# Kernel tuning notes

Measured on AMD Instinct MI355X. Metric: run time of the kernel, lower is better.

## Reference

```python
import jax, jax.numpy as jnp
import numpy as np

N_NODES = 50000
N_EDGES = 800000
DIM = 128
HEADS = 8
DK = DIM // HEADS  # 16
SQRT_DK = float(np.sqrt(DK))


def setup_inputs() -> dict:
    key = jax.random.key(0)
    ks = jax.random.split(key, 12)
    inp = {
        "h": jax.random.normal(ks[0], (N_NODES, DIM), jnp.float32),
        "src": jax.random.randint(ks[1], (N_EDGES,), 0, N_NODES, jnp.int32),
        "dst": jax.random.randint(ks[2], (N_EDGES,), 0, N_NODES, jnp.int32),
        "Wk": jax.random.normal(ks[3], (DIM, DIM), jnp.float32) / np.sqrt(DIM),
        "bk": jnp.zeros((DIM,), jnp.float32),
        "Wq": jax.random.normal(ks[4], (DIM, DIM), jnp.float32) / np.sqrt(DIM),
        "bq": jnp.zeros((DIM,), jnp.float32),
        "Wv": jax.random.normal(ks[5], (DIM, DIM), jnp.float32) / np.sqrt(DIM),
        "bv": jnp.zeros((DIM,), jnp.float32),
        "Wa": jax.random.normal(ks[6], (DIM, DIM), jnp.float32) / np.sqrt(DIM),
        "ba": jnp.zeros((DIM,), jnp.float32),
        "rel_att": jax.random.normal(ks[7], (HEADS, DK, DK), jnp.float32) / np.sqrt(DK),
        "rel_msg": jax.random.normal(ks[8], (HEADS, DK, DK), jnp.float32) / np.sqrt(DK),
        "rel_pri": jnp.ones((HEADS,), jnp.float32),
        "skip": jnp.ones((1,), jnp.float32),
    }
    return inp


def reference(h, src, dst, Wk, bk, Wq, bq, Wv, bv, Wa, ba, rel_att, rel_msg, rel_pri, skip):
    N = h.shape[0]
    # node-level projections -> [N, H, d_k]
    k = (h @ Wk + bk).reshape(N, HEADS, DK)
    q = (h @ Wq + bq).reshape(N, HEADS, DK)
    v = (h @ Wv + bv).reshape(N, HEADS, DK)
    # relation-specific transforms
    k = jnp.einsum('nhi,hij->nhj', k, rel_att)
    v = jnp.einsum('nhi,hij->nhj', v, rel_msg)
    # per-edge score: dot(q[dst], k[src]) over d_k -> [E, H]
    score = jnp.einsum('ehd,ehd->eh', q[dst], k[src]) * rel_pri / SQRT_DK
    # segment softmax over destination nodes (edge_softmax, norm_by='dst')
    smax = jax.ops.segment_max(score, dst, num_segments=N)  # [N, H]
    e = jnp.exp(score - smax[dst])
    ssum = jax.ops.segment_sum(e, dst, num_segments=N)  # [N, H]
    attn = e / ssum[dst]  # [E, H]
    # weighted scatter-sum of messages: sum_e v[src_e] * attn_e -> [N, H, d_k]
    m = v[src] * attn[:, :, None]
    t = jax.ops.segment_sum(m, dst, num_segments=N).reshape(N, DIM)
    # target-specific aggregation (dropout in eval mode = identity, use_norm=False)
    trans_out = t @ Wa + ba
    alpha = jax.nn.sigmoid(skip)  # [1], broadcasts
    new_h = trans_out * alpha + h * (1.0 - alpha)
    return new_h
```

## Files before the change

### kernel.cpp

```cpp
#include <hip/hip_runtime.h>
#include <stdint.h>

#define NN 50000
#define NE 800000

typedef __bf16 v8bf __attribute__((ext_vector_type(8)));
typedef float  v4f  __attribute__((ext_vector_type(4)));
typedef unsigned short v8us __attribute__((ext_vector_type(8)));

#define EXP2F(x) __builtin_amdgcn_exp2f(x)

__device__ __forceinline__ float bf2f(unsigned short u) {
    return __uint_as_float(((unsigned)u) << 16);
}
__device__ __forceinline__ unsigned short f2bf(float f) {
    unsigned u = __float_as_uint(f);
    u += 0x7FFFu + ((u >> 16) & 1u);
    return (unsigned short)(u >> 16);
}
__device__ __forceinline__ float ldf(const void* p, size_t i, int isb) {
    return isb ? bf2f(((const unsigned short*)p)[i]) : ((const float*)p)[i];
}
__device__ __forceinline__ unsigned uminu(unsigned a, unsigned b) {
    return a < b ? a : b;
}

__global__ __launch_bounds__(128) void k_prep(
    const void* __restrict__ Wq, const void* __restrict__ bq,
    const void* __restrict__ Wk, const void* __restrict__ bk,
    const void* __restrict__ Wv, const void* __restrict__ bv,
    const void* __restrict__ Wa, const void* __restrict__ ba,
    const void* __restrict__ rel_att, const void* __restrict__ rel_msg,
    const void* __restrict__ rel_pri, const int* __restrict__ dst,
    unsigned* __restrict__ CNTP, unsigned short* __restrict__ RANKS,
    int* __restrict__ FLAG, unsigned short* __restrict__ WTb,
    float* __restrict__ BC)
{
    int b = blockIdx.x;
    int j = threadIdx.x;
    if (b >= 512) {
        int e = (b - 512) * 128 + j;
        unsigned r = atomicAdd(&CNTP[(unsigned)dst[e] << 4], 1u);
        RANKS[e] = (unsigned short)r;
        return;
    }
    const unsigned rp0 = ((const unsigned*)rel_pri)[0];
    const int isb = ((rp0 & 0xFFFFu) != 0u) ? 1 : 0;
    int m = b >> 7;
    int i = b & 127;
    if (b == 0 && j == 0) FLAG[0] = isb;
    if (m == 0) {
        WTb[((size_t)(0 * 128 + j)) * 128 + i] = f2bf(ldf(Wq, i * 128 + j, isb));
        if (i == 0) BC[j] = ldf(bq, j, isb);
    } else if (m == 3) {
        WTb[((size_t)(3 * 128 + j)) * 128 + i] = f2bf(ldf(Wa, i * 128 + j, isb));
        if (i == 0) BC[3 * 128 + j] = ldf(ba, j, isb);
    } else {
        const void* W    = (m == 1) ? Wk : Wv;
        const void* bias = (m == 1) ? bk : bv;
        const void* R    = (m == 1) ? rel_att : rel_msg;
        int hh = j >> 4, jj = j & 15;
        float scale = (m == 1) ? ldf(rel_pri, hh, isb) * 0.25f : 1.0f;
        float acc = 0.f, bacc = 0.f;
        #pragma unroll
        for (int l = 0; l < 16; ++l) {
            float r = ldf(R, hh * 256 + l * 16 + jj, isb);
            acc  += ldf(W, i * 128 + hh * 16 + l, isb) * r;
            bacc += ldf(bias, hh * 16 + l, isb) * r;
        }
        WTb[((size_t)(m * 128 + j)) * 128 + i] = f2bf(acc * scale);
        if (i == 0) BC[m * 128 + j] = bacc * scale;
    }
}

#define NBG 391
#define NSB 98
__global__ __launch_bounds__(256, 2) void k_qkvscan(
    const void* __restrict__ h, const unsigned short* __restrict__ WTb,
    const float* __restrict__ BC, const int* __restrict__ FLAG,
    unsigned short* __restrict__ Qb, unsigned short* __restrict__ KVb,
    const unsigned* __restrict__ CNTP,
    unsigned* __restrict__ RPS, unsigned* __restrict__ BSUM,
    unsigned* __restrict__ BOFF, unsigned* __restrict__ DONE)
{
    __shared__ __align__(16) unsigned short Ah[128][136];
    __shared__ __align__(16) unsigned short Bh[128][136];
    __shared__ int lastFlag;
    const int tid = threadIdx.x;

    if (blockIdx.x >= NBG) {
        unsigned* shs = (unsigned*)&Ah[0][0];
        int sb = blockIdx.x - NBG;
        int g0 = sb * 512 + tid * 2, g1 = g0 + 1;
        unsigned v0 = (g0 < NN) ? CNTP[(size_t)g0 << 4] : 0u;
        unsigned v1 = (g1 < NN) ? CNTP[(size_t)g1 << 4] : 0u;
        unsigned pv = v0 + v1;
        shs[tid] = pv;
        __syncthreads();
        #pragma unroll
        for (int off = 1; off < 256; off <<= 1) {
            unsigned t = 0;
            if (tid >= off) t = shs[tid - off];
            __syncthreads();
            if (tid >= off) shs[tid] += t;
            __syncthreads();
        }
        unsigned excl = shs[tid] - pv;
        if (g0 < NN) RPS[g0] = excl;
        if (g1 < NN) RPS[g1] = excl + v0;
        if (tid == 255) atomicExch(&BSUM[sb], shs[255]);
        __syncthreads();
        if (tid == 0) {
            __threadfence();
            lastFlag = (atomicAdd(DONE, 1u) == NSB - 1);
        }
        __syncthreads();
        if (!lastFlag) return;
        unsigned bv = (tid < NSB) ? atomicAdd(&BSUM[tid], 0u) : 0u;
        __syncthreads();
        shs[tid] = bv;
        __syncthreads();
        #pragma unroll
        for (int off = 1; off < 256; off <<= 1) {
            unsigned t = 0;
            if (tid >= off) t = shs[tid - off];
            __syncthreads();
            if (tid >= off) shs[tid] += t;
            __syncthreads();
        }
        if (tid < NSB) BOFF[tid] = shs[tid] - bv;
        return;
    }

    const int isb = FLAG[0];
    const int rowBase = blockIdx.x * 128;

    if (isb) {
        #pragma unroll
        for (int i = 0; i < 8; ++i) {
            int lin = tid + i * 256;
            int row = lin >> 4, kc = (lin & 15) * 8;
            int gr = rowBase + row;
            uint4 u = make_uint4(0, 0, 0, 0);
            if (gr < NN) u = *(const uint4*)((const unsigned short*)h + (size_t)gr * 128 + kc);
            *(uint4*)&Ah[row][kc] = u;
        }
    } else {
        #pragma unroll
        for (int i = 0; i < 16; ++i) {
            int lin = tid + i * 256;
            int row = lin >> 5, c4 = (lin & 31) * 4;
            int gr = rowBase + row;
            ushort4 o = make_ushort4(0, 0, 0, 0);
            if (gr < NN) {
                float4 f = *(const float4*)((const float*)h + (size_t)gr * 128 + c4);
                o.x = f2bf(f.x); o.y = f2bf(f.y); o.z = f2bf(f.z); o.w = f2bf(f.w);
            }
            *(ushort4*)&Ah[row][c4] = o;
        }
    }

    const int w = tid >> 6, l = tid & 63;
    const int lr = l & 15, q = l >> 4;
    v4f accK[2][8];

    for (int m = 0; m < 3; ++m) {
        if (m) __syncthreads();
        #pragma unroll
        for (int i = 0; i < 8; ++i) {
            int lin = tid + i * 256;
            int col = lin >> 4, kc = (lin & 15) * 8;
            uint4 u = *(const uint4*)(WTb + ((size_t)(m * 128 + col)) * 128 + kc);
            *(uint4*)&Bh[col][kc] = u;
        }
        __syncthreads();

        v4f acc[2][8];
        #pragma unroll
        for (int rt = 0; rt < 2; ++rt)
            #pragma unroll
            for (int nt = 0; nt < 8; ++nt) {
                float bj = BC[m * 128 + nt * 16 + lr];
                acc[rt][nt] = (v4f){bj, bj, bj, bj};
            }
        #pragma unroll
        for (int kk = 0; kk < 4; ++kk) {
            v8bf a0 = *(const v8bf*)&Ah[w * 32 +  0 + lr][kk * 32 + q * 8];
            v8bf a1 = *(const v8bf*)&Ah[w * 32 + 16 + lr][kk * 32 + q * 8];
            #pragma unroll
            for (int nt = 0; nt < 8; ++nt) {
                v8bf b = *(const v8bf*)&Bh[nt * 16 + lr][kk * 32 + q * 8];
                acc[0][nt] = __builtin_amdgcn_mfma_f32_16x16x32_bf16(a0, b, acc[0][nt], 0, 0, 0);
                acc[1][nt] = __builtin_amdgcn_mfma_f32_16x16x32_bf16(a1, b, acc[1][nt], 0, 0, 0);
            }
        }
        if (m == 0) {
            #pragma unroll
            for (int rt = 0; rt < 2; ++rt)
                #pragma unroll
                for (int nt = 0; nt < 8; ++nt)
                    #pragma unroll
                    for (int r = 0; r < 4; ++r) {
                        int row = rowBase + w * 32 + rt * 16 + q * 4 + r;
                        if (row < NN)
                            Qb[(size_t)row * 128 + nt * 16 + lr] = f2bf(acc[rt][nt][r]);
                    }
        } else if (m == 1) {
            #pragma unroll
            for (int rt = 0; rt < 2; ++rt)
                #pragma unroll
                for (int nt = 0; nt < 8; ++nt) accK[rt][nt] = acc[rt][nt];
        } else {
            #pragma unroll
            for (int rt = 0; rt < 2; ++rt)
                #pragma unroll
                for (int nt = 0; nt < 8; ++nt)
                    #pragma unroll
                    for (int r = 0; r < 4; ++r) {
                        int row = rowBase + w * 32 + rt * 16 + q * 4 + r;
                        if (row < NN) {
                            ushort2 kv;
                            kv.x = f2bf(accK[rt][nt][r]);
                            kv.y = f2bf(acc[rt][nt][r]);
                            *(ushort2*)&KVb[(size_t)row * 256 + (nt * 16 + lr) * 2] = kv;
                        }
                    }
        }
    }
}

__global__ __launch_bounds__(256) void k_fill(
    const int* __restrict__ src, const int* __restrict__ dst,
    const unsigned short* __restrict__ RANKS,
    const unsigned* __restrict__ RPS, const unsigned* __restrict__ BOFF,
    unsigned short* __restrict__ ESRC, unsigned* __restrict__ ROW)
{
    int t = blockIdx.x * 256 + threadIdx.x;
    if (t < NN) ROW[t] = RPS[t] + BOFF[t >> 9];
    if (t >= NE / 2) return;
    int e = t * 2;
    const int2 d2 = *(const int2*)(dst + e);
    const int2 s2 = *(const int2*)(src + e);
    const ushort2 r2 = *(const ushort2*)(RANKS + e);
    unsigned p0 = RPS[d2.x] + BOFF[d2.x >> 9] + r2.x;
    unsigned p1 = RPS[d2.y] + BOFF[d2.y >> 9] + r2.y;
    ESRC[p0] = (unsigned short)s2.x;
    ESRC[p1] = (unsigned short)s2.y;
}

__global__ __launch_bounds__(256) void k_attn(
    const unsigned* __restrict__ ROW,
    const unsigned short* __restrict__ ESRC,
    const unsigned short* __restrict__ Qb, const unsigned short* __restrict__ KVb,
    unsigned short* __restrict__ Tb)
{
    int d = (blockIdx.x * 256 + threadIdx.x) >> 6;
    int lane = threadIdx.x & 63;
    int hl = lane >> 5;
    int sub = lane & 31;
    const float LOG2E = 1.4426950408889634f;

    unsigned beg = ROW[d];
    unsigned end = (d == NN - 1) ? (unsigned)NE : ROW[d + 1];

    const ushort4 qu = *(const ushort4*)(Qb + (size_t)d * 128 + sub * 4);
    float q0 = bf2f(qu.x) * LOG2E, q1 = bf2f(qu.y) * LOG2E;
    float q2 = bf2f(qu.z) * LOG2E, q3 = bf2f(qu.w) * LOG2E;

    float s = 0.f, o0 = 0.f, o1 = 0.f, o2 = 0.f, o3 = 0.f;
    int n = (int)(end - beg);

#define ATT_F(kv) {                                                         \
        float p = q0 * bf2f(kv[0]) + q1 * bf2f(kv[2])                       \
                + q2 * bf2f(kv[4]) + q3 * bf2f(kv[6]);                      \
        p += __shfl_xor(p, 1);                                              \
        p += __shfl_xor(p, 2);                                              \
        float wgt = EXP2F(p);                                               \
        s  += wgt;                                                          \
        o0 += wgt * bf2f(kv[1]); o1 += wgt * bf2f(kv[3]);                   \
        o2 += wgt * bf2f(kv[5]); o3 += wgt * bf2f(kv[7]); }
#define ATT_T(kv, idx) {                                                    \
        float p = q0 * bf2f(kv[0]) + q1 * bf2f(kv[2])                       \
                + q2 * bf2f(kv[4]) + q3 * bf2f(kv[6]);                      \
        p += __shfl_xor(p, 1);                                              \
        p += __shfl_xor(p, 2);                                              \
        float wgt = ((idx) < end) ? EXP2F(p) : 0.f;                         \
        s  += wgt;                                                          \
        o0 += wgt * bf2f(kv[1]); o1 += wgt * bf2f(kv[3]);                   \
        o2 += wgt * bf2f(kv[5]); o3 += wgt * bf2f(kv[7]); }
#define GATH(sid) (*(const v8us*)(KVB + (((unsigned)(sid) << 9) + voff)))

    if (n > 0) {
        const unsigned char* KVB = (const unsigned char*)KVb;
        const unsigned voff = (unsigned)(sub * 16);
        const unsigned last = end - 1;
        const int RT = (n + 7) >> 3;
        const int tail = n & 7;
        const unsigned b0 = beg + (unsigned)hl;

        unsigned sA0 = ESRC[uminu(b0 + 0u, last)];
        unsigned sA1 = ESRC[uminu(b0 + 2u, last)];
        unsigned sA2 = ESRC[uminu(b0 + 4u, last)];
        unsigned sA3 = ESRC[uminu(b0 + 6u, last)];
        v8us kA0 = GATH(sA0), kA1 = GATH(sA1), kA2 = GATH(sA2), kA3 = GATH(sA3);
        unsigned sB0 = 0, sB1 = 0, sB2 = 0, sB3 = 0;
        if (RT > 1) {
            unsigned b1 = b0 + 8u;
            sB0 = ESRC[uminu(b1 + 0u, last)];
            sB1 = ESRC[uminu(b1 + 2u, last)];
            sB2 = ESRC[uminu(b1 + 4u, last)];
            sB3 = ESRC[uminu(b1 + 6u, last)];
        }

        for (int r = 0; r < RT; ++r) {
            v8us kB0 = kA0, kB1 = kA1, kB2 = kA2, kB3 = kA3;
            if (r + 1 < RT) {
                kB0 = GATH(sB0); kB1 = GATH(sB1);
                kB2 = GATH(sB2); kB3 = GATH(sB3);
            }
            unsigned sC0 = sB0, sC1 = sB1, sC2 = sB2, sC3 = sB3;
            if (r + 2 < RT) {
                unsigned b2 = b0 + (unsigned)(8 * (r + 2));
                sC0 = ESRC[uminu(b2 + 0u, last)];
                sC1 = ESRC[uminu(b2 + 2u, last)];
                sC2 = ESRC[uminu(b2 + 4u, last)];
                sC3 = ESRC[uminu(b2 + 6u, last)];
            }
            if (r == RT - 1 && tail) {
                unsigned base = beg + (unsigned)(8 * r) + (unsigned)hl;
                ATT_T(kA0, base + 0u);
                ATT_T(kA1, base + 2u);
                ATT_T(kA2, base + 4u);
                ATT_T(kA3, base + 6u);
            } else {
                ATT_F(kA0); ATT_F(kA1); ATT_F(kA2); ATT_F(kA3);
            }
            kA0 = kB0; kA1 = kB1; kA2 = kB2; kA3 = kB3;
            sB0 = sC0; sB1 = sC1; sB2 = sC2; sB3 = sC3;
        }
    }
#undef ATT_F
#undef ATT_T
#undef GATH

    s  += __shfl_xor(s, 32);
    o0 += __shfl_xor(o0, 32);
    o1 += __shfl_xor(o1, 32);
    o2 += __shfl_xor(o2, 32);
    o3 += __shfl_xor(o3, 32);
    float r = (s > 0.f) ? (1.0f / s) : 0.f;
    if (hl == 0) {
        ushort4 o;
        o.x = f2bf(o0 * r); o.y = f2bf(o1 * r);
        o.z = f2bf(o2 * r); o.w = f2bf(o3 * r);
        *(ushort4*)(Tb + (size_t)d * 128 + sub * 4) = o;
    }
}

__global__ __launch_bounds__(256, 2) void k_final_m(
    const unsigned short* __restrict__ Tb, const unsigned short* __restrict__ WTb,
    const float* __restrict__ BC, const void* __restrict__ h,
    const void* __restrict__ skip, const int* __restrict__ FLAG,
    void* __restrict__ out)
{
    __shared__ __align__(16) unsigned short Ah[128][136];
    __shared__ __align__(16) unsigned short Bh[128][136];
    const int isb = FLAG[0];
    const int tid = threadIdx.x;
    const int rowBase = blockIdx.x * 128;

    #pragma unroll
    for (int i = 0; i < 8; ++i) {
        int lin = tid + i * 256;
        int row = lin >> 4, kc = (lin & 15) * 8;
        int gr = rowBase + row;
        uint4 u = make_uint4(0, 0, 0, 0);
        if (gr < NN) u = *(const uint4*)(Tb + (size_t)gr * 128 + kc);
        *(uint4*)&Ah[row][kc] = u;
    }
    #pragma unroll
    for (int i = 0; i < 8; ++i) {
        int lin = tid + i * 256;
        int col = lin >> 4, kc = (lin & 15) * 8;
        uint4 u = *(const uint4*)(WTb + ((size_t)(3 * 128 + col)) * 128 + kc);
        *(uint4*)&Bh[col][kc] = u;
    }
    __syncthreads();

    const int w = tid >> 6, l = tid & 63;
    const int lr = l & 15, q = l >> 4;
    v4f acc[2][8];
    #pragma unroll
    for (int rt = 0; rt < 2; ++rt)
        #pragma unroll
        for (int nt = 0; nt < 8; ++nt) {
            float bj = BC[3 * 128 + nt * 16 + lr];
            acc[rt][nt] = (v4f){bj, bj, bj, bj};
        }
    #pragma unroll
    for (int kk = 0; kk < 4; ++kk) {
        v8bf a0 = *(const v8bf*)&Ah[w * 32 +  0 + lr][kk * 32 + q * 8];
        v8bf a1 = *(const v8bf*)&Ah[w * 32 + 16 + lr][kk * 32 + q * 8];
        #pragma unroll
        for (int nt = 0; nt < 8; ++nt) {
            v8bf b = *(const v8bf*)&Bh[nt * 16 + lr][kk * 32 + q * 8];
            acc[0][nt] = __builtin_amdgcn_mfma_f32_16x16x32_bf16(a0, b, acc[0][nt], 0, 0, 0);
            acc[1][nt] = __builtin_amdgcn_mfma_f32_16x16x32_bf16(a1, b, acc[1][nt], 0, 0, 0);
        }
    }
    float skipv = ldf(skip, 0, isb);
    float alpha = 1.0f / (1.0f + __expf(-skipv));
    float beta = 1.0f - alpha;
    #pragma unroll
    for (int rt = 0; rt < 2; ++rt)
        #pragma unroll
        for (int nt = 0; nt < 8; ++nt) {
            #pragma unroll
            for (int r = 0; r < 4; ++r) {
                int row = rowBase + w * 32 + rt * 16 + q * 4 + r;
                if (row < NN) {
                    size_t off = (size_t)row * 128 + nt * 16 + lr;
                    float hv = ldf(h, off, isb);
                    float o = alpha * acc[rt][nt][r] + beta * hv;
                    if (isb) ((unsigned short*)out)[off] = f2bf(o);
                    else     ((float*)out)[off] = o;
                }
            }
        }
}

extern "C" void kernel_launch(void* const* d_in, const int* in_sizes, int n_in,
                              void* d_out, int out_size, void* d_ws, size_t ws_size,
                              hipStream_t stream)
{
    const void* h  = d_in[0];
    const int* src = (const int*)d_in[1];
    const int* dst = (const int*)d_in[2];
    const void* Wk = d_in[3];
    const void* bk = d_in[4];
    const void* Wq = d_in[5];
    const void* bq = d_in[6];
    const void* Wv = d_in[7];
    const void* bv = d_in[8];
    const void* Wa = d_in[9];
    const void* ba = d_in[10];
    const void* rel_att = d_in[11];
    const void* rel_msg = d_in[12];
    const void* rel_pri = d_in[13];
    const void* skip    = d_in[14];

    float* F = (float*)d_ws;
    int* FLAG      = (int*)F;
    float* BC      = F + 16;
    unsigned short* WTb = (unsigned short*)(BC + 512);
    unsigned* CNTP = (unsigned*)((float*)(BC + 512) + 32768);
    unsigned* DONE = CNTP + 800000;
    unsigned short* RANKS = (unsigned short*)(DONE + 16);
    unsigned* RPS  = (unsigned*)(RANKS + 800000);
    unsigned* BSUM = RPS + 50048;
    unsigned* BOFF = BSUM + 128;
    unsigned* ROW  = BOFF + 128;
    unsigned short* Tb = (unsigned short*)(ROW + 50048);
    unsigned short* ESRC = Tb + (size_t)NN * 128;
    unsigned short* Qb  = ESRC + NE;
    unsigned short* KVb = Qb + (size_t)NN * 128;

    (void)hipMemsetAsync(CNTP, 0, (800000 + 16) * sizeof(unsigned), stream);

    k_prep<<<512 + 6250, 128, 0, stream>>>(Wq, bq, Wk, bk, Wv, bv, Wa, ba,
                                           rel_att, rel_msg, rel_pri, dst,
                                           CNTP, RANKS, FLAG, WTb, BC);
    k_qkvscan<<<NBG + NSB, 256, 0, stream>>>(h, WTb, BC, FLAG, Qb, KVb,
                                             CNTP, RPS, BSUM, BOFF, DONE);
    k_fill<<<(NE / 2 + 255) / 256, 256, 0, stream>>>(src, dst, RANKS, RPS, BOFF, ESRC, ROW);
    k_attn<<<(NN * 64) / 256, 256, 0, stream>>>(ROW, ESRC, Qb, KVb, Tb);
    k_final_m<<<NBG, 256, 0, stream>>>(Tb, WTb, BC, h, skip, FLAG, d_out);
}
```

Baseline: 249.8 us.

## Replace memset with in-kernel zeroing and overlap degree counting with QKV GEMM

The separate hipMemsetAsync of the count buffer is removed and replaced by extra blocks in the prep kernel that zero it with vector stores. The per-edge destination histogram (atomic rank assignment) moves from the prep kernel into the QKV projection kernel as additional blocks, so it can run alongside the GEMM blocks. The prefix scan becomes its own small kernel launched afterwards. This cuts one API call and overlaps atomic-heavy counting with compute, at the cost of an extra kernel launch and atomics contending with the GEMM for bandwidth.

```diff
diff --git a/kernel.cpp b/kernel.cpp
--- a/kernel.cpp
+++ b/kernel.cpp
@@ -25,23 +25,27 @@
     return a < b ? a : b;
 }
 
-__global__ __launch_bounds__(128) void k_prep(
+__global__ __launch_bounds__(128) void k_prep0(
     const void* __restrict__ Wq, const void* __restrict__ bq,
     const void* __restrict__ Wk, const void* __restrict__ bk,
     const void* __restrict__ Wv, const void* __restrict__ bv,
     const void* __restrict__ Wa, const void* __restrict__ ba,
     const void* __restrict__ rel_att, const void* __restrict__ rel_msg,
-    const void* __restrict__ rel_pri, const int* __restrict__ dst,
-    unsigned* __restrict__ CNTP, unsigned short* __restrict__ RANKS,
+    const void* __restrict__ rel_pri,
+    unsigned* __restrict__ CNTP,
     int* __restrict__ FLAG, unsigned short* __restrict__ WTb,
     float* __restrict__ BC)
 {
     int b = blockIdx.x;
     int j = threadIdx.x;
     if (b >= 512) {
-        int e = (b - 512) * 128 + j;
-        unsigned r = atomicAdd(&CNTP[(unsigned)dst[e] << 4], 1u);
-        RANKS[e] = (unsigned short)r;
+        unsigned idx = (unsigned)(b - 512) * 128u + (unsigned)j;
+        uint4 z = make_uint4(0, 0, 0, 0);
+        #pragma unroll
+        for (int t = 0; t < 25; ++t) {
+            unsigned o = idx + (unsigned)t * 8192u;
+            if (o < 200004u) ((uint4*)CNTP)[o] = z;
+        }
         return;
     }
     const unsigned rp0 = ((const unsigned*)rel_pri)[0];
@@ -74,61 +78,23 @@
 }
 
 #define NBG 391
+#define NHB 3125
 #define NSB 98
-__global__ __launch_bounds__(256, 2) void k_qkvscan(
+__global__ __launch_bounds__(256, 2) void k_qkvh(
     const void* __restrict__ h, const unsigned short* __restrict__ WTb,
     const float* __restrict__ BC, const int* __restrict__ FLAG,
     unsigned short* __restrict__ Qb, unsigned short* __restrict__ KVb,
-    const unsigned* __restrict__ CNTP,
-    unsigned* __restrict__ RPS, unsigned* __restrict__ BSUM,
-    unsigned* __restrict__ BOFF, unsigned* __restrict__ DONE)
+    const int* __restrict__ dst,
+    unsigned* __restrict__ CNTP, unsigned short* __restrict__ RANKS)
 {
     __shared__ __align__(16) unsigned short Ah[128][136];
     __shared__ __align__(16) unsigned short Bh[128][136];
-    __shared__ int lastFlag;
     const int tid = threadIdx.x;
 
     if (blockIdx.x >= NBG) {
-        unsigned* shs = (unsigned*)&Ah[0][0];
-        int sb = blockIdx.x - NBG;
-        int g0 = sb * 512 + tid * 2, g1 = g0 + 1;
-        unsigned v0 = (g0 < NN) ? CNTP[(size_t)g0 << 4] : 0u;
-        unsigned v1 = (g1 < NN) ? CNTP[(size_t)g1 << 4] : 0u;
-        unsigned pv = v0 + v1;
-        shs[tid] = pv;
-        __syncthreads();
-        #pragma unroll
-        for (int off = 1; off < 256; off <<= 1) {
-            unsigned t = 0;
-            if (tid >= off) t = shs[tid - off];
-            __syncthreads();
-            if (tid >= off) shs[tid] += t;
-            __syncthreads();
-        }
-        unsigned excl = shs[tid] - pv;
-        if (g0 < NN) RPS[g0] = excl;
-        if (g1 < NN) RPS[g1] = excl + v0;
-        if (tid == 255) atomicExch(&BSUM[sb], shs[255]);
-        __syncthreads();
-        if (tid == 0) {
-            __threadfence();
-            lastFlag = (atomicAdd(DONE, 1u) == NSB - 1);
-        }
-        __syncthreads();
-        if (!lastFlag) return;
-        unsigned bv = (tid < NSB) ? atomicAdd(&BSUM[tid], 0u) : 0u;
-        __syncthreads();
-        shs[tid] = bv;
-        __syncthreads();
-        #pragma unroll
-        for (int off = 1; off < 256; off <<= 1) {
-            unsigned t = 0;
-            if (tid >= off) t = shs[tid - off];
-            __syncthreads();
-            if (tid >= off) shs[tid] += t;
-            __syncthreads();
-        }
-        if (tid < NSB) BOFF[tid] = shs[tid] - bv;
+        int e = (blockIdx.x - NBG) * 256 + tid;
+        unsigned r = atomicAdd(&CNTP[(unsigned)dst[e] << 4], 1u);
+        RANKS[e] = (unsigned short)r;
         return;
     }
 
@@ -227,6 +193,55 @@
                     }
         }
     }
+}
+
+__global__ __launch_bounds__(256) void k_scan(
+    const unsigned* __restrict__ CNTP,
+    unsigned* __restrict__ RPS, unsigned* __restrict__ BSUM,
+    unsigned* __restrict__ BOFF, unsigned* __restrict__ DONE)
+{
+    __shared__ unsigned shs[256];
+    __shared__ int lastFlag;
+    const int tid = threadIdx.x;
+    int sb = blockIdx.x;
+    int g0 = sb * 512 + tid * 2, g1 = g0 + 1;
+    unsigned v0 = (g0 < NN) ? CNTP[(size_t)g0 << 4] : 0u;
+    unsigned v1 = (g1 < NN) ? CNTP[(size_t)g1 << 4] : 0u;
+    unsigned pv = v0 + v1;
+    shs[tid] = pv;
+    __syncthreads();
+    #pragma unroll
+    for (int off = 1; off < 256; off <<= 1) {
+        unsigned t = 0;
+        if (tid >= off) t = shs[tid - off];
+        __syncthreads();
+        if (tid >= off) shs[tid] += t;
+        __syncthreads();
+    }
+    unsigned excl = shs[tid] - pv;
+    if (g0 < NN) RPS[g0] = excl;
+    if (g1 < NN) RPS[g1] = excl + v0;
+    if (tid == 255) atomicExch(&BSUM[sb], shs[255]);
+    __syncthreads();
+    if (tid == 0) {
+        __threadfence();
+        lastFlag = (atomicAdd(DONE, 1u) == NSB - 1);
+    }
+    __syncthreads();
+    if (!lastFlag) return;
+    unsigned bv = (tid < NSB) ? atomicAdd(&BSUM[tid], 0u) : 0u;
+    __syncthreads();
+    shs[tid] = bv;
+    __syncthreads();
+    #pragma unroll
+    for (int off = 1; off < 256; off <<= 1) {
+        unsigned t = 0;
+        if (tid >= off) t = shs[tid - off];
+        __syncthreads();
+        if (tid >= off) shs[tid] += t;
+        __syncthreads();
+    }
+    if (tid < NSB) BOFF[tid] = shs[tid] - bv;
 }
 
 __global__ __launch_bounds__(256) void k_fill(
@@ -465,13 +480,12 @@
     unsigned short* Qb  = ESRC + NE;
     unsigned short* KVb = Qb + (size_t)NN * 128;
 
-    (void)hipMemsetAsync(CNTP, 0, (800000 + 16) * sizeof(unsigned), stream);
-
-    k_prep<<<512 + 6250, 128, 0, stream>>>(Wq, bq, Wk, bk, Wv, bv, Wa, ba,
-                                           rel_att, rel_msg, rel_pri, dst,
-                                           CNTP, RANKS, FLAG, WTb, BC);
-    k_qkvscan<<<NBG + NSB, 256, 0, stream>>>(h, WTb, BC, FLAG, Qb, KVb,
-                                             CNTP, RPS, BSUM, BOFF, DONE);
+    k_prep0<<<512 + 64, 128, 0, stream>>>(Wq, bq, Wk, bk, Wv, bv, Wa, ba,
+                                          rel_att, rel_msg, rel_pri,
+                                          CNTP, FLAG, WTb, BC);
+    k_qkvh<<<NBG + NHB, 256, 0, stream>>>(h, WTb, BC, FLAG, Qb, KVb,
+                                          dst, CNTP, RANKS);
+    k_scan<<<NSB, 256, 0, stream>>>(CNTP, RPS, BSUM, BOFF, DONE);
     k_fill<<<(NE / 2 + 255) / 256, 256, 0, stream>>>(src, dst, RANKS, RPS, BOFF, ESRC, ROW);
     k_attn<<<(NN * 64) / 256, 256, 0, stream>>>(ROW, ESRC, Qb, KVb, Tb);
     k_final_m<<<NBG, 256, 0, stream>>>(Tb, WTb, BC, h, skip, FLAG, d_out);
```

Result: faster. 241.0 us, median of 2 (-3.5%).
